# Kernel tuning notes

Measured on AMD Instinct MI355X. Metric: run time of the kernel, lower is better.

The kernel has to match this reference:

```python
import jax, jax.numpy as jnp
import numpy as np

SIZE = 11
SIGMA = 1.5
ALPHA = 0.7
K1 = 0.01
K2 = 0.03
DATA_RANGE = 1.0
DN = ('NCDHW', 'OIDHW', 'NCDHW')


def _gauss1d():
    ax = jnp.arange(SIZE, dtype=jnp.float32) - SIZE // 2
    k = jnp.exp(-(ax ** 2) / (2.0 * SIGMA * SIGMA))
    return k / k.sum()


def _blur3d(x, k1):
    # Separable depthwise 3D gaussian blur with zero ('constant') padding.
    # Mathematically identical to the dense 11x11x11 outer-product conv3d
    # in the torch source (zero padding commutes with separable passes).
    ch = x.shape[1]
    pad = SIZE // 2
    for kshape in ((SIZE, 1, 1), (1, SIZE, 1), (1, 1, SIZE)):
        w = jnp.broadcast_to(k1.reshape(1, 1, *kshape), (ch, 1) + kshape)
        pads = [(pad, pad) if s == SIZE else (0, 0) for s in kshape]
        x = jax.lax.conv_general_dilated(
            x, w, window_strides=(1, 1, 1), padding=pads,
            dimension_numbers=DN, feature_group_count=ch)
    return x


def setup_inputs() -> dict:
    key = jax.random.key(0)
    k1, k2 = jax.random.split(key)
    shape = (2, 1, 160, 160, 160)
    pred = jax.random.uniform(k1, shape, dtype=jnp.float32)
    target = jax.random.uniform(k2, shape, dtype=jnp.float32)
    return {"pred": pred, "target": target}


def reference(pred, target):
    k1d = _gauss1d()
    pred32 = pred.astype(jnp.float32)
    target32 = target.astype(jnp.float32)

    # L1
    l1 = jnp.mean(jnp.abs(pred32 - target32))

    # SSIM3D
    mu1 = _blur3d(pred32, k1d)
    mu2 = _blur3d(target32, k1d)
    mu1_sq = mu1 * mu1
    mu2_sq = mu2 * mu2
    mu1_mu2 = mu1 * mu2
    sigma1_sq = _blur3d(pred32 * pred32, k1d) - mu1_sq
    sigma2_sq = _blur3d(target32 * target32, k1d) - mu2_sq
    sigma12 = _blur3d(pred32 * target32, k1d) - mu1_mu2

    C1 = (K1 * DATA_RANGE) ** 2
    C2 = (K2 * DATA_RANGE) ** 2
    ssim_map = ((2.0 * mu1_mu2 + C1) * (2.0 * sigma12 + C2)) / (
        (mu1_sq + mu2_sq + C1) * (sigma1_sq + sigma2_sq + C2) + 1e-12)
    ssim = jnp.mean(ssim_map)

    return ALPHA * l1 + (1.0 - ALPHA) * (1.0 - ssim)
```

## Files before the change

### kernel.cpp

```cpp
#include <hip/hip_runtime.h>

typedef float v2f __attribute__((ext_vector_type(2)));

#define DHW 160
#define PLANE (160*160)
#define VOL (160*160*160)
#define PAD 5
#define KS 11
#define TXW 16
#define TYH 16
#define LZ 32
#define SRX 26
#define SRY 26
#define XA2 18
#define NSLOT 3
#define STAGE_NP (SRY*SRX)
#define NITER ((LZ + 2*PAD) / 2)
#define NBLOCKS 1000
#define CNT_POISON 0xAAAAAAAAu

__device__ __forceinline__ void gauss_w(float w[KS]) {
    float s = 0.f;
#pragma unroll
    for (int i = 0; i < KS; ++i) {
        float d = (float)(i - PAD);
        w[i] = expf(-(d * d) / (2.f * 1.5f * 1.5f));
        s += w[i];
    }
    float inv = 1.f / s;
#pragma unroll
    for (int i = 0; i < KS; ++i) w[i] *= inv;
}

__device__ __forceinline__ float block_reduce(float v, float* sm) {
#pragma unroll
    for (int off = 32; off > 0; off >>= 1)
        v += __shfl_down(v, off);
    int lane = threadIdx.x & 63;
    int wid  = threadIdx.x >> 6;
    if (lane == 0) sm[wid] = v;
    __syncthreads();
    float r = 0.f;
    if (threadIdx.x == 0) r = sm[0] + sm[1] + sm[2] + sm[3];
    return r;
}

__global__ __launch_bounds__(256, 2) void k_fused(
    const float* __restrict__ pred, const float* __restrict__ targ,
    double* __restrict__ accum, unsigned* __restrict__ cnt,
    float* __restrict__ out)
{
    __shared__ __align__(16) v2f   sIn[2][SRY][SRX];
    __shared__ __align__(16) v2f   sXBa[2][SRY][XA2];
    __shared__ __align__(16) v2f   sXBb[2][SRY][XA2];
    __shared__ float sRed[4];

    float gw[KS]; gauss_w(gw);

    const int tile = blockIdx.x;
    const int xt = tile % 10, yt = tile / 10;
    const int z0 = blockIdx.y * LZ;
    const int b  = blockIdx.z;
    const float* __restrict__ P = pred + (size_t)b * VOL;
    const float* __restrict__ T = targ + (size_t)b * VOL;
    const ptrdiff_t dTP = T - P;

    const int tid = threadIdx.x;
    const int tx  = tid & 15;
    const int ty  = tid >> 4;

    const float* sptrP[NSLOT];
    bool sact[NSLOT];
    bool sl1[NSLOT];
#pragma unroll
    for (int i = 0; i < NSLOT; ++i) {
        int idx = tid + 256 * i;
        bool act = idx < STAGE_NP;
        int idc = act ? idx : 0;
        int r   = idc / SRX;
        int c   = idc - r * SRX;
        int gy = yt * TYH + r - PAD;
        int gx = xt * TXW + c - PAD;
        bool inp = (gy >= 0 && gy < DHW && gx >= 0 && gx < DHW);
        sact[i] = act && inp;
        sl1[i]  = act && (r >= PAD && r < PAD + TYH) && (c >= PAD && c < PAD + TXW);
        sptrP[i] = P + (inp ? (gy * DHW + gx) : 0);
    }

    auto stage_fetch = [&](int zz, float vp[NSLOT], float vt[NSLOT]) {
        bool zok = (zz >= 0 && zz < DHW);
        size_t zo = (size_t)(zok ? zz : 0) * PLANE;
#pragma unroll
        for (int i = 0; i < NSLOT; ++i) {
            bool ok = zok && sact[i];
            vp[i] = ok ? sptrP[i][zo] : 0.f;
            vt[i] = ok ? sptrP[i][zo + dTP] : 0.f;
        }
    };
    auto stage_write = [&](int slice, const float vp[NSLOT], const float vt[NSLOT]) {
        v2f* base = &sIn[slice][0][0];
#pragma unroll
        for (int i = 0; i < NSLOT; ++i) {
            int idx = tid + 256 * i;
            if (idx < STAGE_NP) {
                v2f w; w.x = vp[i]; w.y = vt[i];
                base[idx] = w;
            }
        }
    };

    auto xblur_unit = [&](int s, int r4, int cg) {
        const float4* row = (const float4*)&sIn[s][r4][0];
        v2f pt[14];
#pragma unroll
        for (int m2 = 0; m2 < 7; ++m2) {
            float4 q = row[2 * cg + m2];
            v2f lo; lo.x = q.x; lo.y = q.y;
            v2f hi; hi.x = q.z; hi.y = q.w;
            pt[2 * m2]     = lo;
            pt[2 * m2 + 1] = hi;
        }
        v2f sc[14];
#pragma unroll
        for (int i = 0; i < 14; ++i) {
            v2f q = pt[i] * pt[i];
            sc[i].x = q.x + q.y;
            sc[i].y = pt[i].x * pt[i].y;
        }
        v2f aA[4], aB[4];
#pragma unroll
        for (int oo = 0; oo < 4; ++oo) { aA[oo] = 0.f; aB[oo] = 0.f; }
#pragma unroll
        for (int j = 0; j < KS; ++j) {
            float w = gw[j];
#pragma unroll
            for (int oo = 0; oo < 4; ++oo) {
                aA[oo] += pt[oo + j] * w;
                aB[oo] += sc[oo + j] * w;
            }
        }
        float4* wa = (float4*)&sXBa[s][r4][0];
        float4 qa0, qa1;
        qa0.x = aA[0].x; qa0.y = aA[0].y; qa0.z = aA[1].x; qa0.w = aA[1].y;
        qa1.x = aA[2].x; qa1.y = aA[2].y; qa1.z = aA[3].x; qa1.w = aA[3].y;
        wa[2 * cg] = qa0; wa[2 * cg + 1] = qa1;
        float4* wb = (float4*)&sXBb[s][r4][0];
        float4 qb0, qb1;
        qb0.x = aB[0].x; qb0.y = aB[0].y; qb0.z = aB[1].x; qb0.w = aB[1].y;
        qb1.x = aB[2].x; qb1.y = aB[2].y; qb1.z = aB[3].x; qb1.w = aB[3].y;
        wb[2 * cg] = qb0; wb[2 * cg + 1] = qb1;
    };

    v2f pendA[KS], pendB[KS];
#pragma unroll
    for (int j = 0; j < KS; ++j) { pendA[j] = 0.f; pendB[j] = 0.f; }

    float l1s = 0.f, sss = 0.f;
    const float C1 = 0.01f * 0.01f;
    const float C2 = 0.03f * 0.03f;

    auto yblur_push = [&](int s, bool doEmit) {
        v2f tA[KS], tB[KS];
#pragma unroll
        for (int j = 0; j < KS; ++j) {
            tA[j] = sXBa[s][ty + j][tx];
            tB[j] = sXBb[s][ty + j][tx];
        }
        v2f aA, aB; aA = 0.f; aB = 0.f;
#pragma unroll
        for (int j = 0; j < KS; ++j) {
            float w = gw[j];
            aA += tA[j] * w;
            aB += tB[j] * w;
        }
#pragma unroll
        for (int i = 0; i < KS - 1; ++i) {
            float w = gw[10 - i];
            pendA[i] = pendA[i + 1] + aA * w;
            pendB[i] = pendB[i + 1] + aB * w;
        }
        pendA[10] = aA * gw[0];
        pendB[10] = aB * gw[0];
        if (doEmit) {
            v2f mv = pendA[0], ev = pendB[0];
            float mu11 = mv.x * mv.x, mu22 = mv.y * mv.y, mu12 = mv.x * mv.y;
            float musum = mu11 + mu22;
            float s1s2  = ev.x - musum;
            float s12   = ev.y - mu12;
            float num = (2.f * mu12 + C1) * (2.f * s12 + C2);
            float den = (musum + C1) * (s1s2 + C2) + 1e-12f;
            sss += num * __builtin_amdgcn_rcpf(den);
        }
    };

    {
        float vp[NSLOT], vt[NSLOT];
        stage_fetch(z0 - PAD, vp, vt);
        stage_write(0, vp, vt);
        stage_fetch(z0 - PAD + 1, vp, vt);
        stage_write(1, vp, vt);
    }
    __syncthreads();

    for (int m = 0; m < NITER; ++m) {
        const int jA = 2 * m + 2, jB = 2 * m + 3;
        float pA[NSLOT], tAv[NSLOT], pB[NSLOT], tBv[NSLOT];
        const bool doStage = (m < NITER - 1);

        if (doStage) {
            stage_fetch(z0 - PAD + jA, pA, tAv);
            stage_fetch(z0 - PAD + jB, pB, tBv);
            if ((unsigned)(jA - PAD) < (unsigned)LZ) {
#pragma unroll
                for (int i = 0; i < NSLOT; ++i)
                    if (sl1[i]) l1s += fabsf(pA[i] - tAv[i]);
            }
            if ((unsigned)(jB - PAD) < (unsigned)LZ) {
#pragma unroll
                for (int i = 0; i < NSLOT; ++i)
                    if (sl1[i]) l1s += fabsf(pB[i] - tBv[i]);
            }
        }

        if (tid < 208) {
            int s   = (tid >= 104) ? 1 : 0;
            int rem = tid - s * 104;
            xblur_unit(s, rem >> 2, rem & 3);
        }

        __syncthreads();

        if (doStage) {
            stage_write(0, pA, tAv);
            stage_write(1, pB, tBv);
        }

        const bool em = (m >= 5);
        yblur_push(0, em);
        yblur_push(1, em);

        __syncthreads();
    }

    float r1 = block_reduce(l1s, sRed);
    __syncthreads();
    float r2 = block_reduce(sss, sRed);
    if (tid == 0) {
        atomicAdd(&accum[0], (double)r1);
        atomicAdd(&accum[1], (double)r2);
        __threadfence();
        unsigned prev = atomicAdd(cnt, 1u);
        if (prev == CNT_POISON + (unsigned)NBLOCKS - 1u) {
            const double n = 8192000.0;
            double l1   = atomicAdd(&accum[0], 0.0) / n;
            double ssim = atomicAdd(&accum[1], 0.0) / n;
            out[0] = (float)(0.7 * l1 + 0.3 * (1.0 - ssim));
        }
    }
}

extern "C" void kernel_launch(void* const* d_in, const int* in_sizes, int n_in,
                              void* d_out, int out_size, void* d_ws, size_t ws_size,
                              hipStream_t stream) {
    const float* pred = (const float*)d_in[0];
    const float* targ = (const float*)d_in[1];
    float* out = (float*)d_out;
    double* accum = (double*)d_ws;
    unsigned* cnt = (unsigned*)((char*)d_ws + 64);

    dim3 grid(100, DHW / LZ, 2);
    k_fused<<<grid, 256, 0, stream>>>(pred, targ, accum, cnt, out);
}
```

Baseline: 190.2 us.

## Double-buffer LDS stages to software-pipeline x-blur and y-blur with one barrier

Shared staging, x-blur and y-blur buffers gain a parity dimension. Each iteration now runs the x-blur of the current slice pair while the y/z-blur consumes the previous pair's x-blur output. This needs only one __syncthreads per iteration instead of two, and the global loads have more independent work to hide behind. The x-blur thread mapping is also split on a wave boundary (tid<128) so that idle lanes sit in whole waves. In exchange LDS use doubles, which may reduce occupancy below the two-blocks-per-CU launch bound, and one extra pipeline iteration is added to drain.

New measurement: 185.2 us. 2.6% less time.

```diff
diff --git a/kernel.cpp b/kernel.cpp
--- a/kernel.cpp
+++ b/kernel.cpp
@@ -15,7 +15,7 @@
 #define XA2 18
 #define NSLOT 3
 #define STAGE_NP (SRY*SRX)
-#define NITER ((LZ + 2*PAD) / 2)
+#define NBODY 22
 #define NBLOCKS 1000
 #define CNT_POISON 0xAAAAAAAAu
 
@@ -50,9 +50,9 @@
     double* __restrict__ accum, unsigned* __restrict__ cnt,
     float* __restrict__ out)
 {
-    __shared__ __align__(16) v2f   sIn[2][SRY][SRX];
-    __shared__ __align__(16) v2f   sXBa[2][SRY][XA2];
-    __shared__ __align__(16) v2f   sXBb[2][SRY][XA2];
+    __shared__ __align__(16) v2f   sIn [2][2][SRY][SRX];
+    __shared__ __align__(16) v2f   sXBa[2][2][SRY][XA2];
+    __shared__ __align__(16) v2f   sXBb[2][2][SRY][XA2];
     __shared__ float sRed[4];
 
     float gw[KS]; gauss_w(gw);
@@ -97,8 +97,8 @@
             vt[i] = ok ? sptrP[i][zo + dTP] : 0.f;
         }
     };
-    auto stage_write = [&](int slice, const float vp[NSLOT], const float vt[NSLOT]) {
-        v2f* base = &sIn[slice][0][0];
+    auto stage_write = [&](int par, int slice, const float vp[NSLOT], const float vt[NSLOT]) {
+        v2f* base = &sIn[par][slice][0][0];
 #pragma unroll
         for (int i = 0; i < NSLOT; ++i) {
             int idx = tid + 256 * i;
@@ -109,8 +109,8 @@
         }
     };
 
-    auto xblur_unit = [&](int s, int r4, int cg) {
-        const float4* row = (const float4*)&sIn[s][r4][0];
+    auto xblur_unit = [&](int par, int s, int r4, int cg) {
+        const float4* row = (const float4*)&sIn[par][s][r4][0];
         v2f pt[14];
 #pragma unroll
         for (int m2 = 0; m2 < 7; ++m2) {
@@ -139,12 +139,12 @@
                 aB[oo] += sc[oo + j] * w;
             }
         }
-        float4* wa = (float4*)&sXBa[s][r4][0];
+        float4* wa = (float4*)&sXBa[par][s][r4][0];
         float4 qa0, qa1;
         qa0.x = aA[0].x; qa0.y = aA[0].y; qa0.z = aA[1].x; qa0.w = aA[1].y;
         qa1.x = aA[2].x; qa1.y = aA[2].y; qa1.z = aA[3].x; qa1.w = aA[3].y;
         wa[2 * cg] = qa0; wa[2 * cg + 1] = qa1;
-        float4* wb = (float4*)&sXBb[s][r4][0];
+        float4* wb = (float4*)&sXBb[par][s][r4][0];
         float4 qb0, qb1;
         qb0.x = aB[0].x; qb0.y = aB[0].y; qb0.z = aB[1].x; qb0.w = aB[1].y;
         qb1.x = aB[2].x; qb1.y = aB[2].y; qb1.z = aB[3].x; qb1.w = aB[3].y;
@@ -159,12 +159,12 @@
     const float C1 = 0.01f * 0.01f;
     const float C2 = 0.03f * 0.03f;
 
-    auto yblur_push = [&](int s, bool doEmit) {
+    auto yblur_push = [&](int par, int s, bool doEmit) {
         v2f tA[KS], tB[KS];
 #pragma unroll
         for (int j = 0; j < KS; ++j) {
-            tA[j] = sXBa[s][ty + j][tx];
-            tB[j] = sXBb[s][ty + j][tx];
+            tA[j] = sXBa[par][s][ty + j][tx];
+            tB[j] = sXBb[par][s][ty + j][tx];
         }
         v2f aA, aB; aA = 0.f; aB = 0.f;
 #pragma unroll
@@ -193,53 +193,63 @@
         }
     };
 
+    auto body = [&](int i, int par, int parn) {
+        const bool doStage = (i <= 19);
+        const bool doX     = (i <= 20);
+        const bool doY     = (i >= 1);
+        const int  jA = 2 * (i + 1), jB = jA + 1;
+        float pA[NSLOT], tAv[NSLOT], pB[NSLOT], tBv[NSLOT];
+
+        if (doStage) {
+            stage_fetch(z0 - PAD + jA, pA, tAv);
+            stage_fetch(z0 - PAD + jB, pB, tBv);
+        }
+
+        if (doX) {
+            if (tid < 128) {
+                if (tid < 104) xblur_unit(par, 0, tid >> 2, tid & 3);
+            } else {
+                int u = tid - 128;
+                if (u < 104) xblur_unit(par, 1, u >> 2, u & 3);
+            }
+        }
+
+        if (doY) {
+            const bool em = (i >= 6);
+            yblur_push(parn, 0, em);
+            yblur_push(parn, 1, em);
+        }
+
+        if (doStage) {
+            if ((unsigned)(jA - PAD) < (unsigned)LZ) {
+#pragma unroll
+                for (int i2 = 0; i2 < NSLOT; ++i2)
+                    if (sl1[i2]) l1s += fabsf(pA[i2] - tAv[i2]);
+            }
+            if ((unsigned)(jB - PAD) < (unsigned)LZ) {
+#pragma unroll
+                for (int i2 = 0; i2 < NSLOT; ++i2)
+                    if (sl1[i2]) l1s += fabsf(pB[i2] - tBv[i2]);
+            }
+            stage_write(parn, 0, pA, tAv);
+            stage_write(parn, 1, pB, tBv);
+        }
+
+        __syncthreads();
+    };
+
     {
         float vp[NSLOT], vt[NSLOT];
         stage_fetch(z0 - PAD, vp, vt);
-        stage_write(0, vp, vt);
+        stage_write(0, 0, vp, vt);
         stage_fetch(z0 - PAD + 1, vp, vt);
-        stage_write(1, vp, vt);
+        stage_write(0, 1, vp, vt);
     }
     __syncthreads();
 
-    for (int m = 0; m < NITER; ++m) {
-        const int jA = 2 * m + 2, jB = 2 * m + 3;
-        float pA[NSLOT], tAv[NSLOT], pB[NSLOT], tBv[NSLOT];
-        const bool doStage = (m < NITER - 1);
-
-        if (doStage) {
-            stage_fetch(z0 - PAD + jA, pA, tAv);
-            stage_fetch(z0 - PAD + jB, pB, tBv);
-            if ((unsigned)(jA - PAD) < (unsigned)LZ) {
-#pragma unroll
-                for (int i = 0; i < NSLOT; ++i)
-                    if (sl1[i]) l1s += fabsf(pA[i] - tAv[i]);
-            }
-            if ((unsigned)(jB - PAD) < (unsigned)LZ) {
-#pragma unroll
-                for (int i = 0; i < NSLOT; ++i)
-                    if (sl1[i]) l1s += fabsf(pB[i] - tBv[i]);
-            }
-        }
-
-        if (tid < 208) {
-            int s   = (tid >= 104) ? 1 : 0;
-            int rem = tid - s * 104;
-            xblur_unit(s, rem >> 2, rem & 3);
-        }
-
-        __syncthreads();
-
-        if (doStage) {
-            stage_write(0, pA, tAv);
-            stage_write(1, pB, tBv);
-        }
-
-        const bool em = (m >= 5);
-        yblur_push(0, em);
-        yblur_push(1, em);
-
-        __syncthreads();
+    for (int ii = 0; ii < NBODY / 2; ++ii) {
+        body(2 * ii,     0, 1);
+        body(2 * ii + 1, 1, 0);
     }
 
     float r1 = block_reduce(l1s, sRed);
```
